# Kernel optimization log

Hardware: AMD Instinct MI355X
Metric: run time of the kernel (lower is better)

The kernel has to match this reference:

```python
import jax, jax.numpy as jnp
import numpy as np

N_NODES = 100000
N_EDGES = 1600000
N_GRAPHS = 64
HID = 128
N_EXPERTS = 8
IN_DIM = 4


def setup_inputs() -> dict:
    key = jax.random.key(0)
    ks = jax.random.split(key, 12)
    atomic_numbers = jax.random.uniform(ks[0], (N_NODES,), dtype=jnp.float32) * 80.0
    pos = jax.random.normal(ks[1], (N_NODES, 3), dtype=jnp.float32)
    edge_index = jax.random.randint(ks[2], (2, N_EDGES), 0, N_NODES, dtype=jnp.int64)
    batch = jnp.sort(jax.random.randint(ks[3], (N_NODES,), 0, N_GRAPHS, dtype=jnp.int64))
    s1 = 1.0 / np.sqrt(IN_DIM)
    s2 = 1.0 / np.sqrt(HID)
    W1 = jax.random.uniform(ks[4], (IN_DIM, HID), jnp.float32, -s1, s1)
    b1 = jnp.zeros((HID,), jnp.float32)
    W2 = jax.random.uniform(ks[5], (HID, HID), jnp.float32, -s2, s2)
    b2 = jnp.zeros((HID,), jnp.float32)
    Wlin = jax.random.uniform(ks[6], (HID, N_EXPERTS), jnp.float32, -s2, s2)
    blin = jax.random.uniform(ks[7], (N_EXPERTS,), jnp.float32, -s2, s2)
    return {"atomic_numbers": atomic_numbers, "pos": pos, "edge_index": edge_index,
            "batch": batch, "W1": W1, "b1": b1, "W2": W2, "b2": b2,
            "Wlin": Wlin, "blin": blin}


def _gcn_conv(x, W, b, src, dst, deg_inv_sqrt, n_nodes):
    # PyG GCNConv: x' = W x; aggregate deg^-1/2[src]*deg^-1/2[dst] * x'[src] into dst; + bias
    h = x @ W  # [N, out]
    norm = deg_inv_sqrt[src] * deg_inv_sqrt[dst]  # [E+N]
    msg = h[src] * norm[:, None]  # gathered, normalized messages
    out = jax.ops.segment_sum(msg, dst, num_segments=n_nodes)
    return out + b


def reference(atomic_numbers, pos, edge_index, batch, W1, b1, W2, b2, Wlin, blin):
    n = atomic_numbers.shape[0]
    x = jnp.concatenate([atomic_numbers[:, None], pos], axis=-1)  # [N, 4]
    # add self-loops (GCNConv default add_self_loops=True)
    loop = jnp.arange(n, dtype=edge_index.dtype)
    src = jnp.concatenate([edge_index[0], loop])
    dst = jnp.concatenate([edge_index[1], loop])
    deg = jax.ops.segment_sum(jnp.ones_like(dst, dtype=jnp.float32), dst, num_segments=n)
    deg_inv_sqrt = jnp.where(deg > 0, jax.lax.rsqrt(jnp.maximum(deg, 1e-12)), 0.0)
    x = _gcn_conv(x, W1, b1, src, dst, deg_inv_sqrt, n)
    x = jax.nn.relu(x)
    # dropout p=0.5 is identity in eval mode
    x = _gcn_conv(x, W2, b2, src, dst, deg_inv_sqrt, n)
    x = x @ Wlin + blin  # [N, num_experts]
    # global_mean_pool over graph ids
    sums = jax.ops.segment_sum(x, batch, num_segments=N_GRAPHS)
    cnts = jax.ops.segment_sum(jnp.ones((n,), jnp.float32), batch, num_segments=N_GRAPHS)
    pooled = sums / jnp.maximum(cnts, 1.0)[:, None]
    return jax.nn.log_softmax(pooled, axis=1)
```

## Files before the change

### kernel.cpp

```cpp
#include <hip/hip_runtime.h>
#include <math.h>

#define HID 128
#define NEXP 8
#define NGRAPH 64
#define EPC 2048
#define MAXB 512
#define NXC 8
#define NREP 8
#define NPS 8

__device__ inline unsigned short f2bf(float f) {
    unsigned u = __float_as_uint(f);
    u += 0x7FFF + ((u >> 16) & 1);
    return (unsigned short)(u >> 16);
}
__device__ inline unsigned packbf(float lo, float hi) {
    return (unsigned)f2bf(lo) | ((unsigned)f2bf(hi) << 16);
}
__device__ inline float bflo(unsigned u) { return __uint_as_float(u << 16); }
__device__ inline float bfhi(unsigned u) { return __uint_as_float(u & 0xFFFF0000u); }

__global__ void k_init0(float* __restrict__ pool, float* __restrict__ pcnt,
                        const float* __restrict__ W2, const float* __restrict__ Wlin,
                        const float* __restrict__ b2, float* __restrict__ C,
                        float* __restrict__ bb2, int* __restrict__ gcur8,
                        int mregions, int capx) {
    int i = blockIdx.x * 256 + threadIdx.x;
    if (i < mregions) gcur8[i] = i * capx;
    if (i < NREP * NGRAPH * NEXP) pool[i] = 0.0f;
    if (i < NREP * NGRAPH) pcnt[i] = 0.0f;
    int ci = i - NREP * NGRAPH * NEXP;
    if (ci >= 0 && ci < HID * NEXP) {
        int k = ci >> 3, j = ci & 7;
        float s = 0.0f;
        for (int m = 0; m < HID; m++) s += W2[k * HID + m] * Wlin[m * NEXP + j];
        C[ci] = s;
    }
    int bi = ci - HID * NEXP;
    if (bi >= 0 && bi < NEXP) {
        float s = 0.0f;
        for (int m = 0; m < HID; m++) s += b2[m] * Wlin[m * NEXP + bi];
        bb2[bi] = s;
    }
}

__global__ void __launch_bounds__(256) k_binA(
        const int* __restrict__ src, const int* __restrict__ dst,
        int* __restrict__ gcur8, unsigned* __restrict__ binned, int e, int nbuck) {
    __shared__ int h0[MAXB];
    __shared__ int h1[MAXB];
    __shared__ int lstart[MAXB];
    __shared__ int lcur[MAXB];
    __shared__ int gbase[MAXB];
    __shared__ int wtot[4];
    __shared__ unsigned packed[EPC];
    __shared__ unsigned short sbkt[EPC];
    int c = blockIdx.x, t = threadIdx.x;
    int w = t >> 6, lane = t & 63;
    int x = c & (NXC - 1);
    int start = c * EPC;
    int m = e - start < EPC ? e - start : EPC;

    int d[8], sv[8];
    if (m == EPC) {
        int4 da = ((const int4*)(dst + start))[2 * t];
        int4 db = ((const int4*)(dst + start))[2 * t + 1];
        int4 sa = ((const int4*)(src + start))[2 * t];
        int4 sb = ((const int4*)(src + start))[2 * t + 1];
        d[0] = da.x; d[1] = da.y; d[2] = da.z; d[3] = da.w;
        d[4] = db.x; d[5] = db.y; d[6] = db.z; d[7] = db.w;
        sv[0] = sa.x; sv[1] = sa.y; sv[2] = sa.z; sv[3] = sa.w;
        sv[4] = sb.x; sv[5] = sb.y; sv[6] = sb.z; sv[7] = sb.w;
    } else {
#pragma unroll
        for (int j = 0; j < 8; j++) {
            int idx = t * 8 + j;
            if (idx < m) { d[j] = dst[start + idx]; sv[j] = src[start + idx]; }
        }
    }
    int* hm = (w < 2) ? h0 : h1;
    h0[t] = 0; h0[t + 256] = 0;
    h1[t] = 0; h1[t + 256] = 0;
    __syncthreads();
#pragma unroll
    for (int j = 0; j < 8; j++)
        if (t * 8 + j < m) atomicAdd(&hm[d[j] >> 8], 1);
    __syncthreads();
    int v0 = h0[2 * t] + h1[2 * t];
    int v1 = h0[2 * t + 1] + h1[2 * t + 1];
    int sum = v0 + v1;
    int incl = sum;
#pragma unroll
    for (int dd = 1; dd < 64; dd <<= 1) {
        int y = __shfl_up(incl, dd, 64);
        if (lane >= dd) incl += y;
    }
    if (lane == 63) wtot[w] = incl;
    __syncthreads();
    int pre = 0;
#pragma unroll
    for (int ww = 0; ww < 4; ww++) pre += (ww < w) ? wtot[ww] : 0;
    int ex = pre + incl - sum;
    lstart[2 * t] = ex;     lstart[2 * t + 1] = ex + v0;
    lcur[2 * t]   = ex;     lcur[2 * t + 1]   = ex + v0;
    for (int b = t; b < nbuck; b += 256) {
        int hv = h0[b] + h1[b];
        gbase[b] = hv ? atomicAdd(&gcur8[b * NXC + x], hv) : 0;
    }
    __syncthreads();
#pragma unroll
    for (int j = 0; j < 8; j++) {
        if (t * 8 + j < m) {
            int b = d[j] >> 8;
            int p = atomicAdd(&lcur[b], 1);
            packed[p] = ((unsigned)(d[j] & 255) << 24) | (unsigned)sv[j];
            sbkt[p] = (unsigned short)b;
        }
    }
    __syncthreads();
    for (int idx = t; idx < m; idx += 256) {
        int b = sbkt[idx];
        binned[gbase[b] + (idx - lstart[b])] = packed[idx];
    }
}

__global__ void k_binB(const unsigned* __restrict__ binned, const int* __restrict__ gcur8,
                       const float* __restrict__ an, const float* __restrict__ pos,
                       int* __restrict__ cnt, int* __restrict__ off,
                       float* __restrict__ dinv, float4* __restrict__ xs,
                       int* __restrict__ eidx, int n, int capx) {
    __shared__ int h[256];
    __shared__ int cur[256];
    __shared__ int wtot[4];
    int b = blockIdx.x, t = threadIdx.x;
    int w = t >> 6, lane = t & 63;
    int cbase = b * NXC;
    int ob = cbase * capx;
    h[t] = 0;
    __syncthreads();
#pragma unroll
    for (int x = 0; x < NXC; x++) {
        int rs = (cbase + x) * capx, re = gcur8[cbase + x];
        for (int k = rs + t; k < re; k += 256)
            atomicAdd(&h[binned[k] >> 24], 1);
    }
    __syncthreads();
    int v = h[t];
    int incl = v;
#pragma unroll
    for (int dd = 1; dd < 64; dd <<= 1) {
        int y = __shfl_up(incl, dd, 64);
        if (lane >= dd) incl += y;
    }
    if (lane == 63) wtot[w] = incl;
    __syncthreads();
    int pre = 0;
#pragma unroll
    for (int ww = 0; ww < 4; ww++) pre += (ww < w) ? wtot[ww] : 0;
    int ex = pre + incl - v;
    cur[t] = ex;
    int node = (b << 8) + t;
    if (node < n) {
        float di = rsqrtf((float)v + 1.0f);
        cnt[node]  = v;
        off[node]  = ob + ex;
        dinv[node] = di;
        xs[node] = make_float4(an[node] * di, pos[3 * node] * di,
                               pos[3 * node + 1] * di, pos[3 * node + 2] * di);
    }
    __syncthreads();
#pragma unroll
    for (int x = 0; x < NXC; x++) {
        int rs = (cbase + x) * capx, re = gcur8[cbase + x];
        for (int k = rs + t; k < re; k += 256) {
            unsigned u = binned[k];
            int p = atomicAdd(&cur[u >> 24], 1);
            eidx[ob + p] = (int)(u & 0xFFFFFF);
        }
    }
}

__global__ void k_gxz(const float4* __restrict__ xs, const int* __restrict__ eidx,
                      const int* __restrict__ off, const int* __restrict__ cnt,
                      const float* __restrict__ dinv, const float* __restrict__ W1,
                      const float* __restrict__ b1, const float* __restrict__ C,
                      uint4* __restrict__ z, int n) {
    int tid = blockIdx.x * 256 + threadIdx.x;
    int i = tid >> 1;
    int par = tid & 1;
    if (i >= n) return;
    float4 a = par ? make_float4(0.f, 0.f, 0.f, 0.f) : xs[i];
    int o = off[i], c = cnt[i];
    int k = par;
    for (; k + 6 < c; k += 8) {
        int i0 = eidx[o + k],     i1 = eidx[o + k + 2];
        int i2 = eidx[o + k + 4], i3 = eidx[o + k + 6];
        float4 v0 = xs[i0], v1 = xs[i1], v2 = xs[i2], v3 = xs[i3];
        a.x += v0.x + v1.x + v2.x + v3.x;
        a.y += v0.y + v1.y + v2.y + v3.y;
        a.z += v0.z + v1.z + v2.z + v3.z;
        a.w += v0.w + v1.w + v2.w + v3.w;
    }
    for (; k < c; k += 2) {
        float4 v0 = xs[eidx[o + k]];
        a.x += v0.x; a.y += v0.y; a.z += v0.z; a.w += v0.w;
    }
    a.x += __shfl_xor(a.x, 1, 64);
    a.y += __shfl_xor(a.y, 1, 64);
    a.z += __shfl_xor(a.z, 1, 64);
    a.w += __shfl_xor(a.w, 1, 64);
    float di = dinv[i];
    float z0 = 0.f, z1 = 0.f, z2 = 0.f, z3 = 0.f,
          z4 = 0.f, z5 = 0.f, z6 = 0.f, z7 = 0.f;
#pragma unroll 4
    for (int kk = 0; kk < HID; kk++) {
        float x1k = fmaxf(di * (a.x * W1[kk] + a.y * W1[HID + kk] +
                                a.z * W1[2 * HID + kk] + a.w * W1[3 * HID + kk])
                          + b1[kk], 0.0f);
        const float* cr = C + kk * NEXP;
        z0 += x1k * cr[0]; z1 += x1k * cr[1];
        z2 += x1k * cr[2]; z3 += x1k * cr[3];
        z4 += x1k * cr[4]; z5 += x1k * cr[5];
        z6 += x1k * cr[6]; z7 += x1k * cr[7];
    }
    if (par == 0) {
        uint4 outv;
        outv.x = packbf(z0 * di, z1 * di);
        outv.y = packbf(z2 * di, z3 * di);
        outv.z = packbf(z4 * di, z5 * di);
        outv.w = packbf(z6 * di, z7 * di);
        z[i] = outv;
    }
}

__global__ void k_gz(const uint4* __restrict__ z4, const int* __restrict__ eidx,
                     const int* __restrict__ off, const int* __restrict__ cnt,
                     const float* __restrict__ dinv, const int* __restrict__ batch,
                     float* __restrict__ pool, float* __restrict__ pcnt, int n) {
    int t = threadIdx.x;
    int slot = t >> 4;
    int l = t & 15;
    int i0 = blockIdx.x * (16 * NPS) + slot * NPS;
    if (i0 >= n) return;
    int i1 = i0 + NPS < n ? i0 + NPS : n;
    int rep = (blockIdx.x + slot) & (NREP - 1);
    float* rp  = pool + (size_t)rep * NGRAPH * NEXP;
    float* rpc = pcnt + (size_t)rep * NGRAPH;
    int Q = l >> 2;

    int curg = -1;
    float r0 = 0.0f, r1 = 0.0f, runlen = 0.0f;
    for (int i = i0; i < i1; i++) {
        float a0 = 0.f, a1 = 0.f, a2 = 0.f, a3 = 0.f,
              a4 = 0.f, a5 = 0.f, a6 = 0.f, a7 = 0.f;
        int o = off[i], c = cnt[i];
        for (int k = l; k < c; k += 16) {
            uint4 zr = z4[eidx[o + k]];
            a0 += bflo(zr.x); a1 += bfhi(zr.x);
            a2 += bflo(zr.y); a3 += bfhi(zr.y);
            a4 += bflo(zr.z); a5 += bfhi(zr.z);
            a6 += bflo(zr.w); a7 += bfhi(zr.w);
        }
        if (l == 0) {
            uint4 zr = z4[i];
            a0 += bflo(zr.x); a1 += bfhi(zr.x);
            a2 += bflo(zr.y); a3 += bfhi(zr.y);
            a4 += bflo(zr.z); a5 += bfhi(zr.z);
            a6 += bflo(zr.w); a7 += bfhi(zr.w);
        }
        a0 += __shfl_xor(a0, 8, 64); a1 += __shfl_xor(a1, 8, 64);
        a2 += __shfl_xor(a2, 8, 64); a3 += __shfl_xor(a3, 8, 64);
        a4 += __shfl_xor(a4, 8, 64); a5 += __shfl_xor(a5, 8, 64);
        a6 += __shfl_xor(a6, 8, 64); a7 += __shfl_xor(a7, 8, 64);
        a0 += __shfl_xor(a0, 4, 64); a1 += __shfl_xor(a1, 4, 64);
        a2 += __shfl_xor(a2, 4, 64); a3 += __shfl_xor(a3, 4, 64);
        a4 += __shfl_xor(a4, 4, 64); a5 += __shfl_xor(a5, 4, 64);
        a6 += __shfl_xor(a6, 4, 64); a7 += __shfl_xor(a7, 4, 64);
        float r0v, r1v;
        switch (Q) {
            case 0:  r0v = a0; r1v = a1; break;
            case 1:  r0v = a2; r1v = a3; break;
            case 2:  r0v = a4; r1v = a5; break;
            default: r0v = a6; r1v = a7; break;
        }
        r0v += __shfl_xor(r0v, 1, 64); r1v += __shfl_xor(r1v, 1, 64);
        r0v += __shfl_xor(r0v, 2, 64); r1v += __shfl_xor(r1v, 2, 64);
        float di = dinv[i];
        float v0 = di * r0v, v1 = di * r1v;
        int g = batch[i];
        if (g != curg) {
            if (curg >= 0 && (l & 3) == 0) {
                atomicAdd(&rp[curg * NEXP + 2 * Q], r0);
                atomicAdd(&rp[curg * NEXP + 2 * Q + 1], r1);
                if (l == 0) atomicAdd(&rpc[curg], runlen);
            }
            curg = g; r0 = v0; r1 = v1; runlen = 1.0f;
        } else { r0 += v0; r1 += v1; runlen += 1.0f; }
    }
    if (curg >= 0 && (l & 3) == 0) {
        atomicAdd(&rp[curg * NEXP + 2 * Q], r0);
        atomicAdd(&rp[curg * NEXP + 2 * Q + 1], r1);
        if (l == 0) atomicAdd(&rpc[curg], runlen);
    }
}

__global__ void k_lsm(const float* __restrict__ pool, const float* __restrict__ pcnt,
                      const float* __restrict__ blin, const float* __restrict__ bb2,
                      float* __restrict__ out) {
    int g = threadIdx.x;
    if (g >= NGRAPH) return;
    float p[NEXP];
#pragma unroll
    for (int k = 0; k < NEXP; k++) p[k] = 0.0f;
    float cg = 0.0f;
#pragma unroll
    for (int rr = 0; rr < NREP; rr++) {
#pragma unroll
        for (int k = 0; k < NEXP; k++) p[k] += pool[rr * NGRAPH * NEXP + g * NEXP + k];
        cg += pcnt[rr * NGRAPH + g];
    }
    float inv = 1.0f / fmaxf(cg, 1.0f);
    float v[NEXP], m = -1e30f;
#pragma unroll
    for (int k = 0; k < NEXP; k++) {
        v[k] = p[k] * inv + blin[k] + bb2[k];
        m = fmaxf(m, v[k]);
    }
    float s = 0.0f;
#pragma unroll
    for (int k = 0; k < NEXP; k++) s += expf(v[k] - m);
    float ls = logf(s);
#pragma unroll
    for (int k = 0; k < NEXP; k++) out[g * NEXP + k] = v[k] - m - ls;
}

extern "C" void kernel_launch(void* const* d_in, const int* in_sizes, int n_in,
                              void* d_out, int out_size, void* d_ws, size_t ws_size,
                              hipStream_t stream) {
    const float* an   = (const float*)d_in[0];
    const float* pos  = (const float*)d_in[1];
    const int*   ei   = (const int*)d_in[2];
    const int*   batch= (const int*)d_in[3];
    const float* W1   = (const float*)d_in[4];
    const float* b1   = (const float*)d_in[5];
    const float* W2   = (const float*)d_in[6];
    const float* b2   = (const float*)d_in[7];
    const float* Wlin = (const float*)d_in[8];
    const float* blin = (const float*)d_in[9];
    float* out = (float*)d_out;

    const int n = in_sizes[0];
    const int e = in_sizes[2] / 2;
    const int* src = ei;
    const int* dst = ei + e;

    const int nbuck = (n + 255) >> 8;
    const int ch    = (e + EPC - 1) / EPC;
    const int mreg  = nbuck * NXC;
    const int capx  = 2 * (e / (mreg > 0 ? mreg : 1)) + 256;

    char* p = (char*)d_ws;
    float4* xs    = (float4*)p;       p += sizeof(float4) * (size_t)n;
    uint4*  z     = (uint4*)p;        p += sizeof(uint4) * (size_t)n;
    float* C      = (float*)p;        p += sizeof(float) * HID * NEXP;
    float* bb2    = (float*)p;        p += sizeof(float) * NEXP;
    float* dinv   = (float*)p;        p += sizeof(float) * (size_t)n;
    float* pool   = (float*)p;        p += sizeof(float) * NREP * NGRAPH * NEXP;
    float* pcnt   = (float*)p;        p += sizeof(float) * NREP * NGRAPH;
    int*   cnt    = (int*)p;          p += sizeof(int) * (size_t)n;
    int*   off    = (int*)p;          p += sizeof(int) * (size_t)n;
    int*   gcur8  = (int*)p;          p += sizeof(int) * (mreg + 8);
    unsigned* binned = (unsigned*)p;  p += sizeof(unsigned) * (size_t)mreg * capx;
    int*   eidx   = (int*)p;          p += sizeof(int) * (size_t)mreg * capx;

    const int initN = NREP * NGRAPH * NEXP + HID * NEXP + NEXP;
    const int initG = initN > mreg ? initN : mreg;
    k_init0<<<(initG + 255) / 256, 256, 0, stream>>>(pool, pcnt, W2, Wlin, b2, C,
                                                     bb2, gcur8, mreg, capx);
    k_binA<<<ch, 256, 0, stream>>>(src, dst, gcur8, binned, e, nbuck);
    k_binB<<<nbuck, 256, 0, stream>>>(binned, gcur8, an, pos, cnt, off, dinv,
                                      xs, eidx, n, capx);

    k_gxz<<<(2 * n + 255) / 256, 256, 0, stream>>>(xs, eidx, off, cnt, dinv,
                                                   W1, b1, C, z, n);

    k_gz<<<(n + 16 * NPS - 1) / (16 * NPS), 256, 0, stream>>>(z, eidx, off, cnt, dinv,
                                                              batch, pool, pcnt, n);
    k_lsm<<<1, 64, 0, stream>>>(pool, pcnt, blin, bb2, out);
}
```

Measured before the change: 196.9 us.

## Split CSR build blocks into node halves and double edge chunk size

k_binB now launches two blocks per 256-node bucket. Each block handles a 128-node half, filtering the bucket's binned edges by the high bit of the local node id and writing into its own half of the eidx region. k_binA processes 4096 edges per block instead of 2048, loading 16 edges per thread. The aim is more parallelism in the scatter stage and fewer binning blocks with fewer global atomics. The cost is that each binned entry is read twice, and each half relies on its edge count fitting within four sub-region capacities.

```diff
diff --git a/kernel.cpp b/kernel.cpp
--- a/kernel.cpp
+++ b/kernel.cpp
@@ -4,11 +4,12 @@
 #define HID 128
 #define NEXP 8
 #define NGRAPH 64
-#define EPC 2048
+#define EPC 4096
 #define MAXB 512
 #define NXC 8
 #define NREP 8
 #define NPS 8
+#define HALF 128
 
 __device__ inline unsigned short f2bf(float f) {
     unsigned u = __float_as_uint(f);
@@ -62,20 +63,23 @@
     int start = c * EPC;
     int m = e - start < EPC ? e - start : EPC;
 
-    int d[8], sv[8];
+    int d[16], sv[16];
     if (m == EPC) {
-        int4 da = ((const int4*)(dst + start))[2 * t];
-        int4 db = ((const int4*)(dst + start))[2 * t + 1];
-        int4 sa = ((const int4*)(src + start))[2 * t];
-        int4 sb = ((const int4*)(src + start))[2 * t + 1];
-        d[0] = da.x; d[1] = da.y; d[2] = da.z; d[3] = da.w;
-        d[4] = db.x; d[5] = db.y; d[6] = db.z; d[7] = db.w;
-        sv[0] = sa.x; sv[1] = sa.y; sv[2] = sa.z; sv[3] = sa.w;
-        sv[4] = sb.x; sv[5] = sb.y; sv[6] = sb.z; sv[7] = sb.w;
+        const int4* d4 = (const int4*)(dst + start);
+        const int4* s4 = (const int4*)(src + start);
+#pragma unroll
+        for (int q = 0; q < 4; q++) {
+            int4 dd4 = d4[4 * t + q];
+            int4 ss4 = s4[4 * t + q];
+            d[4 * q + 0] = dd4.x; d[4 * q + 1] = dd4.y;
+            d[4 * q + 2] = dd4.z; d[4 * q + 3] = dd4.w;
+            sv[4 * q + 0] = ss4.x; sv[4 * q + 1] = ss4.y;
+            sv[4 * q + 2] = ss4.z; sv[4 * q + 3] = ss4.w;
+        }
     } else {
 #pragma unroll
-        for (int j = 0; j < 8; j++) {
-            int idx = t * 8 + j;
+        for (int j = 0; j < 16; j++) {
+            int idx = t * 16 + j;
             if (idx < m) { d[j] = dst[start + idx]; sv[j] = src[start + idx]; }
         }
     }
@@ -84,8 +88,8 @@
     h1[t] = 0; h1[t + 256] = 0;
     __syncthreads();
 #pragma unroll
-    for (int j = 0; j < 8; j++)
-        if (t * 8 + j < m) atomicAdd(&hm[d[j] >> 8], 1);
+    for (int j = 0; j < 16; j++)
+        if (t * 16 + j < m) atomicAdd(&hm[d[j] >> 8], 1);
     __syncthreads();
     int v0 = h0[2 * t] + h1[2 * t];
     int v1 = h0[2 * t + 1] + h1[2 * t + 1];
@@ -110,8 +114,8 @@
     }
     __syncthreads();
 #pragma unroll
-    for (int j = 0; j < 8; j++) {
-        if (t * 8 + j < m) {
+    for (int j = 0; j < 16; j++) {
+        if (t * 16 + j < m) {
             int b = d[j] >> 8;
             int p = atomicAdd(&lcur[b], 1);
             packed[p] = ((unsigned)(d[j] & 255) << 24) | (unsigned)sv[j];
@@ -130,44 +134,50 @@
                        int* __restrict__ cnt, int* __restrict__ off,
                        float* __restrict__ dinv, float4* __restrict__ xs,
                        int* __restrict__ eidx, int n, int capx) {
-    __shared__ int h[256];
-    __shared__ int cur[256];
-    __shared__ int wtot[4];
-    int b = blockIdx.x, t = threadIdx.x;
-    int w = t >> 6, lane = t & 63;
+    __shared__ int h[HALF];
+    __shared__ int cur[HALF];
+    __shared__ int wtot[2];
+    int bh = blockIdx.x, t = threadIdx.x;
+    int b = bh >> 1, half = bh & 1;
     int cbase = b * NXC;
-    int ob = cbase * capx;
-    h[t] = 0;
+    int hb = cbase * capx + half * (NXC / 2) * capx;
+    if (t < HALF) h[t] = 0;
     __syncthreads();
 #pragma unroll
     for (int x = 0; x < NXC; x++) {
         int rs = (cbase + x) * capx, re = gcur8[cbase + x];
-        for (int k = rs + t; k < re; k += 256)
-            atomicAdd(&h[binned[k] >> 24], 1);
-    }
-    __syncthreads();
-    int v = h[t];
-    int incl = v;
-#pragma unroll
-    for (int dd = 1; dd < 64; dd <<= 1) {
-        int y = __shfl_up(incl, dd, 64);
-        if (lane >= dd) incl += y;
-    }
-    if (lane == 63) wtot[w] = incl;
-    __syncthreads();
-    int pre = 0;
-#pragma unroll
-    for (int ww = 0; ww < 4; ww++) pre += (ww < w) ? wtot[ww] : 0;
-    int ex = pre + incl - v;
-    cur[t] = ex;
-    int node = (b << 8) + t;
-    if (node < n) {
-        float di = rsqrtf((float)v + 1.0f);
-        cnt[node]  = v;
-        off[node]  = ob + ex;
-        dinv[node] = di;
-        xs[node] = make_float4(an[node] * di, pos[3 * node] * di,
-                               pos[3 * node + 1] * di, pos[3 * node + 2] * di);
+        for (int k = rs + t; k < re; k += 256) {
+            int f = (int)(binned[k] >> 24);
+            if ((f >> 7) == half) atomicAdd(&h[f & (HALF - 1)], 1);
+        }
+    }
+    __syncthreads();
+    int v = 0, ex = 0;
+    if (t < HALF) {
+        int lane = t & 63, w = t >> 6;
+        v = h[t];
+        int incl = v;
+#pragma unroll
+        for (int dd = 1; dd < 64; dd <<= 1) {
+            int y = __shfl_up(incl, dd, 64);
+            if (lane >= dd) incl += y;
+        }
+        if (lane == 63) wtot[w] = incl;
+        ex = incl - v;
+    }
+    __syncthreads();
+    if (t < HALF) {
+        if (t >= 64) ex += wtot[0];
+        cur[t] = ex;
+        int node = (b << 8) + half * HALF + t;
+        if (node < n) {
+            float di = rsqrtf((float)v + 1.0f);
+            cnt[node]  = v;
+            off[node]  = hb + ex;
+            dinv[node] = di;
+            xs[node] = make_float4(an[node] * di, pos[3 * node] * di,
+                                   pos[3 * node + 1] * di, pos[3 * node + 2] * di);
+        }
     }
     __syncthreads();
 #pragma unroll
@@ -175,8 +185,11 @@
         int rs = (cbase + x) * capx, re = gcur8[cbase + x];
         for (int k = rs + t; k < re; k += 256) {
             unsigned u = binned[k];
-            int p = atomicAdd(&cur[u >> 24], 1);
-            eidx[ob + p] = (int)(u & 0xFFFFFF);
+            int f = (int)(u >> 24);
+            if ((f >> 7) == half) {
+                int p = atomicAdd(&cur[f & (HALF - 1)], 1);
+                eidx[hb + p] = (int)(u & 0xFFFFFF);
+            }
         }
     }
 }
@@ -379,8 +392,8 @@
     k_init0<<<(initG + 255) / 256, 256, 0, stream>>>(pool, pcnt, W2, Wlin, b2, C,
                                                      bb2, gcur8, mreg, capx);
     k_binA<<<ch, 256, 0, stream>>>(src, dst, gcur8, binned, e, nbuck);
-    k_binB<<<nbuck, 256, 0, stream>>>(binned, gcur8, an, pos, cnt, off, dinv,
-                                      xs, eidx, n, capx);
+    k_binB<<<2 * nbuck, 256, 0, stream>>>(binned, gcur8, an, pos, cnt, off, dinv,
+                                          xs, eidx, n, capx);
 
     k_gxz<<<(2 * n + 255) / 256, 256, 0, stream>>>(xs, eidx, off, cnt, dinv,
                                                    W1, b1, C, z, n);
```

Result: faster. 178.7 us (-9.2%).
